# Optimization experiments

Hardware: AMD Instinct MI355X
Metric: run time of the kernel (lower is better)

The kernel has to match this reference:

```python
import jax, jax.numpy as jnp
import numpy as np

N_OER, N_CONCEPT, N_CLASS = 100000, 20000, 1000
F_ENT, HID = 64, 128
E_SR, E_EP, E_COV, E_BEL = 200000, 400000, 400000, 100000
NEG_SLOPE = 0.2


def _edges(k, n_src, n_dst, e):
    k1, k2 = jax.random.split(k)
    return jnp.stack([jax.random.randint(k1, (e,), 0, n_src),
                      jax.random.randint(k2, (e,), 0, n_dst)]).astype(jnp.int32)


def setup_inputs() -> dict:
    key = jax.random.key(0)
    ks = jax.random.split(key, 24)
    s = 0.05  # small init scale for numerically stable attention logits
    inp = {
        'x_oer': jax.random.normal(ks[0], (N_OER, F_ENT), jnp.float32),
        'x_concept': jax.random.normal(ks[1], (N_CONCEPT, F_ENT), jnp.float32),
        'x_class': jax.random.normal(ks[2], (N_CLASS, F_ENT), jnp.float32),
        'e_oer': jax.random.uniform(ks[3], (N_OER, F_ENT), jnp.float32),
        'e_concept': jax.random.uniform(ks[4], (N_CONCEPT, F_ENT), jnp.float32),
        'e_class': jax.random.uniform(ks[5], (N_CLASS, F_ENT), jnp.float32),
        'W_lin': jax.random.normal(ks[6], (3, F_ENT, HID), jnp.float32) * s,
        'b_lin': jnp.zeros((3, HID), jnp.float32),
        'Wsrc': jax.random.normal(ks[7], (2, 5, HID, HID), jnp.float32) * s,
        'Wdst': jax.random.normal(ks[8], (2, 5, HID, HID), jnp.float32) * s,
        'att_src': jax.random.normal(ks[9], (2, 5, HID), jnp.float32) * s,
        'att_dst': jax.random.normal(ks[10], (2, 5, HID), jnp.float32) * s,
        'b_gat': jnp.zeros((2, 5, HID), jnp.float32),
        'W_cls': jax.random.normal(ks[11], (2 * (F_ENT + HID), 1), jnp.float32) * s,
        'b_cls': jnp.zeros((1,), jnp.float32),
        'ei_before_sr': _edges(ks[12], N_OER, N_OER, E_SR),
        'ei_covers': _edges(ks[14], N_OER, N_CONCEPT, E_COV),
        'ei_belongs': _edges(ks[15], N_CONCEPT, N_CLASS, E_BEL),
        'ei_rev_covers': _edges(ks[16], N_CONCEPT, N_OER, E_COV),
        'ei_rev_belongs': _edges(ks[17], N_CLASS, N_CONCEPT, E_BEL),
    }
    # before_ep edges guaranteed self-loop-free (PyG removes then re-adds self loops)
    k1, k2 = jax.random.split(ks[13])
    src = jax.random.randint(k1, (E_EP,), 0, N_OER)
    dst = (src + jax.random.randint(k2, (E_EP,), 1, N_OER)) % N_OER
    inp['ei_before_ep'] = jnp.stack([src, dst]).astype(jnp.int32)
    return inp


def _gat(x_src, x_dst, src, dst, Ws, Wd, a_s, a_d, b, n_dst):
    # PyG GATConv, heads=1: h = xW (no bias); alpha = softmax_dst(leaky_relu(a_s.h_s[i] + a_d.h_d[j]))
    h_s = x_src @ Ws                                   # [Ns, C]
    h_d = x_dst @ Wd                                   # [Nd, C]
    logit = jax.nn.leaky_relu((h_s @ a_s)[src] + (h_d @ a_d)[dst], NEG_SLOPE)  # [E]
    m = jax.ops.segment_max(logit, dst, num_segments=n_dst)
    ex = jnp.exp(logit - m[dst])
    denom = jax.ops.segment_sum(ex, dst, num_segments=n_dst)
    alpha = ex / denom[dst]
    out = jax.ops.segment_sum(h_s[src] * alpha[:, None], dst, num_segments=n_dst)
    return out + b


def _forward(x_oer, x_concept, x_class, e_oer, e_concept, e_class,
             W_lin, b_lin, Wsrc, Wdst, att_src, att_dst, b_gat, W_cls, b_cls,
             ei_before_sr, ei_before_ep, ei_covers, ei_belongs,
             ei_rev_covers, ei_rev_belongs):
    # per-node-type input projection of the random embeddings
    h_oer = e_oer @ W_lin[0] + b_lin[0]
    h_con = e_concept @ W_lin[1] + b_lin[1]
    h_cls = e_class @ W_lin[2] + b_lin[2]

    # add self loops for OER->OER 'before_ep' (add_self_loops=True)
    loop = jnp.arange(N_OER, dtype=jnp.int32)
    ep_src = jnp.concatenate([ei_before_ep[0], loop])
    ep_dst = jnp.concatenate([ei_before_ep[1], loop])

    for l in range(2):
        P = lambda r: (Wsrc[l, r], Wdst[l, r], att_src[l, r], att_dst[l, r], b_gat[l, r])
        o_ep = _gat(h_oer, h_oer, ep_src, ep_dst, *P(0), N_OER)
        o_cov = _gat(h_oer, h_con, ei_covers[0], ei_covers[1], *P(1), N_CONCEPT)
        o_bel = _gat(h_con, h_cls, ei_belongs[0], ei_belongs[1], *P(2), N_CLASS)
        o_rcov = _gat(h_con, h_oer, ei_rev_covers[0], ei_rev_covers[1], *P(3), N_OER)
        o_rbel = _gat(h_cls, h_con, ei_rev_belongs[0], ei_rev_belongs[1], *P(4), N_CONCEPT)
        # HeteroConv aggr='mean' over edge types per destination node type
        h_oer = (o_ep + o_rcov) * 0.5
        h_con = (o_cov + o_rbel) * 0.5
        h_cls = o_bel

    n_oer = jnp.concatenate([x_oer, h_oer], axis=1)          # [N_OER, F_ENT+HID]
    feat = jnp.concatenate([n_oer[ei_before_sr[0]], n_oer[ei_before_sr[1]]], axis=1)
    return (feat @ W_cls + b_cls)[:, 0]                      # [E_SR]


def reference(x_oer, x_concept, x_class, e_oer, e_concept, e_class,
              W_lin, b_lin, Wsrc, Wdst, att_src, att_dst, b_gat, W_cls, b_cls,
              ei_before_sr, ei_before_ep, ei_covers, ei_belongs,
              ei_rev_covers, ei_rev_belongs):
    return _forward(x_oer, x_concept, x_class, e_oer, e_concept, e_class,
                    W_lin, b_lin, Wsrc, Wdst, att_src, att_dst, b_gat, W_cls, b_cls,
                    ei_before_sr, ei_before_ep, ei_covers, ei_belongs,
                    ei_rev_covers, ei_rev_belongs)
```

## Files before the change

### kernel.cpp

```cpp
#include <hip/hip_runtime.h>
#include <hip/hip_bf16.h>

#define NOER 100000
#define NCON 20000
#define NCLS 1000
#define FENT 64
#define HID 128
#define ESR 200000
#define EEP 400000
#define ECOV 400000
#define EBEL 100000
#define NEG 0.2f
#define NB_TOT 121000

#define SL0 0
#define SL1 NOER
#define SL2 (2*NOER)
#define SL3 (2*NOER + NCON)
#define SL4 (2*NOER + 2*NCON)
#define SL_TOT (2*NOER + 2*NCON + NCLS)
#define DL0 0
#define DL1 NOER
#define DL2 (NOER + NCON)
#define DL3 (NOER + NCON + NCLS)
#define DL4 (2*NOER + NCON + NCLS)
#define DL_TOT (2*NOER + 2*NCON + NCLS)
#define EX_TOT 1500000
#define SCAN_B1 ((DL_TOT + 255) / 256)

typedef unsigned short u16;
typedef unsigned int u32;
typedef short v8s __attribute__((ext_vector_type(8)));
typedef float v4f __attribute__((ext_vector_type(4)));

__device__ __forceinline__ float b2f(u32 bits) { return __uint_as_float(bits << 16); }
__device__ __forceinline__ u16 f2b(float x) {
    __hip_bfloat16 h = __float2bfloat16(x);
    return *(u16*)&h;
}
__device__ __forceinline__ float wredsum(float p) {
#pragma unroll
    for (int off = 32; off; off >>= 1) p += __shfl_down(p, off);
    return p;
}

__device__ __forceinline__ void edge_decode(int e, const int* __restrict__ ep,
                                            const int* __restrict__ cov,
                                            const int* __restrict__ bel,
                                            const int* __restrict__ rcov,
                                            const int* __restrict__ rbel,
                                            int& s, int& g) {
    if (e < 500000) {
        if (e < EEP) { s = ep[e]; g = DL0 + ep[EEP + e]; }
        else { s = e - EEP; g = DL0 + s; }
    } else if (e < 900000)  { int i = e - 500000;  s = cov[i];  g = DL1 + cov[ECOV + i]; }
    else if (e < 1000000)   { int i = e - 900000;  s = bel[i];  g = DL2 + bel[EBEL + i]; }
    else if (e < 1400000)   { int i = e - 1000000; s = rcov[i]; g = DL3 + rcov[ECOV + i]; }
    else                    { int i = e - 1400000; s = rbel[i]; g = DL4 + rbel[EBEL + i]; }
}

__global__ void k_count(const int* __restrict__ ep, const int* __restrict__ cov,
                        const int* __restrict__ bel, const int* __restrict__ rcov,
                        const int* __restrict__ rbel, int* __restrict__ counts) {
    int e = blockIdx.x * blockDim.x + threadIdx.x;
    if (e >= EX_TOT) return;
    int s, g;
    edge_decode(e, ep, cov, bel, rcov, rbel, s, g);
    atomicAdd(counts + g, 1);
}

__global__ void k_scan1(const int* __restrict__ counts, int* __restrict__ part,
                        int* __restrict__ bsum) {
    __shared__ int sm[256];
    int i = blockIdx.x * 256 + threadIdx.x;
    int v = (i < DL_TOT) ? counts[i] : 0;
    sm[threadIdx.x] = v;
    __syncthreads();
#pragma unroll
    for (int off = 1; off < 256; off <<= 1) {
        int x = (threadIdx.x >= off) ? sm[threadIdx.x - off] : 0;
        __syncthreads();
        sm[threadIdx.x] += x;
        __syncthreads();
    }
    if (i < DL_TOT) part[i] = sm[threadIdx.x];
    if (threadIdx.x == 255) bsum[blockIdx.x] = sm[255];
}

__global__ void k_scan2(int* __restrict__ bsum) {
    __shared__ int sm[1024];
    int t = threadIdx.x;
    sm[t] = (t < SCAN_B1) ? bsum[t] : 0;
    __syncthreads();
#pragma unroll
    for (int off = 1; off < 1024; off <<= 1) {
        int x = (t >= off) ? sm[t - off] : 0;
        __syncthreads();
        sm[t] += x;
        __syncthreads();
    }
    if (t < SCAN_B1) bsum[t] = sm[t];
}

__global__ void k_scan3(const int* __restrict__ part, const int* __restrict__ bsum,
                        const int* __restrict__ counts, int* __restrict__ S,
                        int* __restrict__ cursor) {
    int i = blockIdx.x * 256 + threadIdx.x;
    if (i >= DL_TOT) return;
    int b = blockIdx.x;
    int s = part[i] + (b > 0 ? bsum[b - 1] : 0);
    S[i] = s;
    cursor[i] = s - counts[i];
}

__global__ void k_fill(const int* __restrict__ ep, const int* __restrict__ cov,
                       const int* __restrict__ bel, const int* __restrict__ rcov,
                       const int* __restrict__ rbel, int* __restrict__ cursor,
                       int* __restrict__ csr) {
    int e = blockIdx.x * blockDim.x + threadIdx.x;
    if (e >= EX_TOT) return;
    int s, g;
    edge_decode(e, ep, cov, bel, rcov, rbel, s, g);
    int pos = atomicAdd(cursor + g, 1);
    csr[pos] = s;
}

__device__ __forceinline__ int deg_bin(int d) { int b = d > 63 ? 63 : d; return 63 - b; }

__global__ void k_hist2(const int* __restrict__ counts, int* __restrict__ bh) {
    __shared__ int lh[64];
    if (threadIdx.x < 64) lh[threadIdx.x] = 0;
    __syncthreads();
    int g = blockIdx.x * 256 + threadIdx.x;
    if (g < DL_TOT) atomicAdd(&lh[deg_bin(counts[g])], 1);
    __syncthreads();
    if (threadIdx.x < 64) bh[threadIdx.x * SCAN_B1 + blockIdx.x] = lh[threadIdx.x];
}

__global__ void k_bscan(const int* __restrict__ bh, int* __restrict__ boff,
                        int* __restrict__ bintot) {
    __shared__ int sm[256];
    __shared__ int carry;
    int bin = blockIdx.x;
    if (threadIdx.x == 0) carry = 0;
    __syncthreads();
    for (int c0 = 0; c0 < SCAN_B1; c0 += 256) {
        int i = c0 + threadIdx.x;
        int v = (i < SCAN_B1) ? bh[bin * SCAN_B1 + i] : 0;
        sm[threadIdx.x] = v;
        __syncthreads();
#pragma unroll
        for (int off = 1; off < 256; off <<= 1) {
            int x = (threadIdx.x >= off) ? sm[threadIdx.x - off] : 0;
            __syncthreads();
            sm[threadIdx.x] += x;
            __syncthreads();
        }
        if (i < SCAN_B1) boff[bin * SCAN_B1 + i] = carry + sm[threadIdx.x] - v;
        __syncthreads();
        if (threadIdx.x == 255) carry += sm[255];
        __syncthreads();
    }
    if (threadIdx.x == 0) bintot[bin] = carry;
}

__global__ void k_hscan(const int* __restrict__ hist, int* __restrict__ bcur) {
    int t = threadIdx.x;
    int h = hist[t];
    int v = h;
#pragma unroll
    for (int off = 1; off < 64; off <<= 1) {
        int x = __shfl_up(v, off);
        if (t >= off) v += x;
    }
    bcur[t] = v - h;
}

__global__ void k_perm2(const int* __restrict__ counts, const int* __restrict__ binbase,
                        const int* __restrict__ boff, int* __restrict__ perm) {
    __shared__ int lh[64];
    if (threadIdx.x < 64)
        lh[threadIdx.x] = binbase[threadIdx.x] + boff[threadIdx.x * SCAN_B1 + blockIdx.x];
    __syncthreads();
    int g = blockIdx.x * 256 + threadIdx.x;
    if (g >= DL_TOT) return;
    int pos = atomicAdd(&lh[deg_bin(counts[g])], 1);
    perm[pos] = g;
}

__global__ void k_cast(const float* __restrict__ e_oer, const float* __restrict__ e_con,
                       const float* __restrict__ e_cls, u16* __restrict__ eb) {
    int idx = blockIdx.x * blockDim.x + threadIdx.x;
    int i4 = idx * 4;
    if (i4 >= NB_TOT * FENT) return;
    const float* src;
    if (i4 < 6400000) src = e_oer + i4;
    else if (i4 < 7680000) src = e_con + (i4 - 6400000);
    else src = e_cls + (i4 - 7680000);
    float4 v = *(const float4*)src;
    u16* d = eb + i4;
    d[0] = f2b(v.x); d[1] = f2b(v.y); d[2] = f2b(v.z); d[3] = f2b(v.w);
}

__global__ void k_prep(const float* __restrict__ W_lin, const float* __restrict__ Wsrc,
                       const float* __restrict__ b_gat,
                       u16* __restrict__ Wlt, u16* __restrict__ Woer, u16* __restrict__ Wcon,
                       u16* __restrict__ Wcls, float* __restrict__ boer,
                       float* __restrict__ bcon, float* __restrict__ bcls2) {
    int i = blockIdx.x * 256 + threadIdx.x;
    if (i < 24576) {
        int t = i / 8192, r = i % 8192, c = r >> 6, k = r & 63;
        Wlt[i] = f2b(W_lin[t * 8192 + k * 128 + c]);
        return;
    }
    i -= 24576;
    if (i < 65536) {
        int l = i >> 15, r = i & 32767, c = r >> 8, k2 = r & 255;
        int rel = 5 * l + (k2 < 128 ? 0 : 3), k = k2 & 127;
        Woer[i] = f2b(Wsrc[(size_t)rel * 16384 + k * 128 + c]);
        return;
    }
    i -= 65536;
    if (i < 65536) {
        int l = i >> 15, r = i & 32767, c = r >> 8, k2 = r & 255;
        int rel = 5 * l + (k2 < 128 ? 1 : 4), k = k2 & 127;
        Wcon[i] = f2b(Wsrc[(size_t)rel * 16384 + k * 128 + c]);
        return;
    }
    i -= 65536;
    if (i < 32768) {
        int l = i >> 14, r = i & 16383, c = r >> 7, k = r & 127;
        Wcls[i] = f2b(Wsrc[(size_t)(5 * l + 2) * 16384 + k * 128 + c]);
        return;
    }
    i -= 32768;
    if (i < 256) { int l = i >> 7, c = i & 127;
        boer[i] = 0.5f * (b_gat[(5 * l + 0) * 128 + c] + b_gat[(5 * l + 3) * 128 + c]); return; }
    i -= 256;
    if (i < 256) { int l = i >> 7, c = i & 127;
        bcon[i] = 0.5f * (b_gat[(5 * l + 1) * 128 + c] + b_gat[(5 * l + 4) * 128 + c]); return; }
    i -= 256;
    if (i < 256) { int l = i >> 7, c = i & 127;
        bcls2[i] = b_gat[(5 * l + 2) * 128 + c]; }
}

__global__ void k_wvec(const float* __restrict__ Wsrc, const float* __restrict__ as_,
                       const float* __restrict__ Wdst, const float* __restrict__ ad,
                       float* __restrict__ wsv, float* __restrict__ wdv) {
    int a = blockIdx.x >> 5;
    int r = ((blockIdx.x & 31) << 2) + (threadIdx.x >> 6);
    int lane = threadIdx.x & 63;
    const float *W, *v;
    float* o;
    if (a < 10) { W = Wsrc + (size_t)a * HID * HID; v = as_ + a * HID; o = wsv + a * HID; }
    else { W = Wdst + (size_t)(a - 10) * HID * HID; v = ad + (a - 10) * HID; o = wdv + (a - 10) * HID; }
    float p = W[r * HID + lane] * v[lane] + W[r * HID + 64 + lane] * v[64 + lane];
    p = wredsum(p);
    if (lane == 0) o[r] = p;
}

struct GemmJob {
    const u16* A0;
    const u16* A1;
    const u16* Wt;
    const float* bias;
    float scale;
    int n, K;
    u16* out;
};

__global__ __launch_bounds__(256) void k_mgemm(GemmJob j0, GemmJob j1, GemmJob j2,
                                               int nb0, int nb1) {
    __shared__ u16 lA[64][40];
    __shared__ u16 lB[128][40];
    GemmJob J;
    int b = blockIdx.x;
    if (b < nb0) J = j0;
    else if (b < nb0 + nb1) { J = j1; b -= nb0; }
    else { J = j2; b -= nb0 + nb1; }
    const int row0 = b * 64;
    const int tid = threadIdx.x, lane = tid & 63, w = tid >> 6;
    const int wr = w >> 1, wc = w & 1;
    const int fr = lane & 15, kg = lane >> 4;
    const int astride = J.A1 ? 128 : J.K;
    v4f acc[2][4];
#pragma unroll
    for (int i = 0; i < 2; ++i)
#pragma unroll
        for (int c = 0; c < 4; ++c) acc[i][c] = (v4f){0.f, 0.f, 0.f, 0.f};

    for (int k0 = 0; k0 < J.K; k0 += 32) {
        const u16* Asrc; int kk;
        if (k0 < 128) { Asrc = J.A0; kk = k0; } else { Asrc = J.A1; kk = k0 - 128; }
        __syncthreads();
        {
            int r = tid >> 2, seg = tid & 3;
            int gr = row0 + r;
            uint4 u = make_uint4(0u, 0u, 0u, 0u);
            if (gr < J.n) u = *(const uint4*)(Asrc + (size_t)gr * astride + kk + seg * 8);
            *(uint4*)&lA[r][seg * 8] = u;
        }
#pragma unroll
        for (int i = 0; i < 2; ++i) {
            int m = tid * 2 + i, c = m >> 2, seg = m & 3;
            uint4 u = *(const uint4*)(J.Wt + (size_t)c * J.K + k0 + seg * 8);
            *(uint4*)&lB[c][seg * 8] = u;
        }
        __syncthreads();
        v8s a0 = *(const v8s*)&lA[32 * wr + fr][8 * kg];
        v8s a1 = *(const v8s*)&lA[32 * wr + 16 + fr][8 * kg];
#pragma unroll
        for (int c = 0; c < 4; ++c) {
            v8s bf = *(const v8s*)&lB[64 * wc + 16 * c + fr][8 * kg];
            acc[0][c] = __builtin_amdgcn_mfma_f32_16x16x32_bf16(a0, bf, acc[0][c], 0, 0, 0);
            acc[1][c] = __builtin_amdgcn_mfma_f32_16x16x32_bf16(a1, bf, acc[1][c], 0, 0, 0);
        }
    }
#pragma unroll
    for (int i = 0; i < 2; ++i)
#pragma unroll
        for (int c = 0; c < 4; ++c) {
            int col = 64 * wc + 16 * c + fr;
            float bv = J.bias[col];
#pragma unroll
            for (int jj = 0; jj < 4; ++jj) {
                int gr = row0 + 32 * wr + 16 * i + 4 * kg + jj;
                if (gr < J.n) J.out[(size_t)gr * 128 + col] = f2b(acc[i][c][jj] * J.scale + bv);
            }
        }
}

__global__ void k_dots_all(const u16* __restrict__ hb, const float* __restrict__ wsv,
                           const float* __restrict__ wdv, float* __restrict__ slp,
                           float* __restrict__ dlp, int lb) {
    int t = blockIdx.x * blockDim.x + threadIdx.x;
    int n = t >> 6, lane = t & 63;
    if (n >= NB_TOT) return;
    const u32* h;
    int m;
    const float *v0, *v1, *v2, *v3;
    float *o0, *o1, *o2, *o3;
    if (n < NOER) {
        m = n; h = (const u32*)hb;
        v0 = wsv + (lb + 0) * HID; o0 = slp + SL0 + m;
        v1 = wsv + (lb + 1) * HID; o1 = slp + SL1 + m;
        v2 = wdv + (lb + 0) * HID; o2 = dlp + DL0 + m;
        v3 = wdv + (lb + 3) * HID; o3 = dlp + DL3 + m;
    } else if (n < NOER + NCON) {
        m = n - NOER; h = (const u32*)(hb + (size_t)NOER * HID);
        v0 = wsv + (lb + 2) * HID; o0 = slp + SL2 + m;
        v1 = wsv + (lb + 3) * HID; o1 = slp + SL3 + m;
        v2 = wdv + (lb + 1) * HID; o2 = dlp + DL1 + m;
        v3 = wdv + (lb + 4) * HID; o3 = dlp + DL4 + m;
    } else {
        m = n - NOER - NCON; h = (const u32*)(hb + (size_t)(NOER + NCON) * HID);
        v0 = wsv + (lb + 4) * HID; o0 = slp + SL4 + m;
        v1 = wdv + (lb + 2) * HID; o1 = dlp + DL2 + m;
        v2 = nullptr; o2 = nullptr; v3 = nullptr; o3 = nullptr;
    }
    u32 hu = h[(size_t)m * 64 + lane];
    float h0 = b2f(hu & 0xffffu), h1 = b2f(hu >> 16);
    float p0 = 0.f, p1 = 0.f, p2 = 0.f, p3 = 0.f;
    { float2 a = *(const float2*)(v0 + 2 * lane); p0 = h0 * a.x + h1 * a.y; }
    { float2 a = *(const float2*)(v1 + 2 * lane); p1 = h0 * a.x + h1 * a.y; }
    if (v2) { float2 a = *(const float2*)(v2 + 2 * lane); p2 = h0 * a.x + h1 * a.y; }
    if (v3) { float2 a = *(const float2*)(v3 + 2 * lane); p3 = h0 * a.x + h1 * a.y; }
    p0 = wredsum(p0); p1 = wredsum(p1); p2 = wredsum(p2); p3 = wredsum(p3);
    if (lane == 0) {
        o0[0] = p0; o1[0] = p1;
        if (o2) o2[0] = p2;
        if (o3) o3[0] = p3;
    }
}

__global__ __launch_bounds__(256) void k_agg_all(const int* __restrict__ csr,
                                                 const int* __restrict__ S,
                                                 const int* __restrict__ perm,
                                                 const float* __restrict__ slp,
                                                 const float* __restrict__ dlp,
                                                 const u16* __restrict__ hb,
                                                 u16* __restrict__ tmp) {
    int gi = blockIdx.x * 16 + (threadIdx.x >> 4);
    if (gi >= DL_TOT) return;
    int g = perm[gi];
    int lane = threadIdx.x & 63;
    int ks = lane & 15;
    int grpbase = lane & 48;
    int c4 = ks * 4;
    const u32* h;
    int sb;
    if (g < DL1)      { h = (const u32*)hb; sb = SL0; }
    else if (g < DL2) { h = (const u32*)hb; sb = SL1; }
    else if (g < DL3) { h = (const u32*)(hb + (size_t)NOER * HID); sb = SL2; }
    else if (g < DL4) { h = (const u32*)(hb + (size_t)NOER * HID); sb = SL3; }
    else              { h = (const u32*)(hb + (size_t)(NOER + NCON) * HID); sb = SL4; }
    int beg = (g == 0) ? 0 : S[g - 1];
    int end = S[g];
    float dlv = dlp[g];
    const u32* hc = h + c4;
    float acc[8] = {};
    float denp = 0.f;
    for (int c0 = beg; c0 < end; c0 += 16) {
        int nch = end - c0;
        if (nch > 16) nch = 16;
        int s_l = 0;
        float ex_l = 0.f;
        if (ks < nch) {
            s_l = csr[c0 + ks];
            float lg = slp[sb + s_l] + dlv;
            lg = lg > 0.f ? lg : NEG * lg;
            ex_l = __expf(lg);
            denp += ex_l;
        }
        uint4 hu[16];
#pragma unroll
        for (int j = 0; j < 16; ++j) {
            if (j < nch) {
                int s = __shfl(s_l, grpbase + j);
                hu[j] = *(const uint4*)(hc + ((size_t)s << 6));
            }
        }
#pragma unroll
        for (int j = 0; j < 16; ++j) {
            if (j < nch) {
                float ex = __shfl(ex_l, grpbase + j);
#pragma unroll
                for (int q = 0; q < 4; ++q) {
                    u32 w = ((const u32*)&hu[j])[q];
                    acc[2 * q]     = fmaf(ex, __uint_as_float(w << 16), acc[2 * q]);
                    acc[2 * q + 1] = fmaf(ex, __uint_as_float(w & 0xffff0000u), acc[2 * q + 1]);
                }
            }
        }
    }
    denp += __shfl_xor(denp, 8);
    denp += __shfl_xor(denp, 4);
    denp += __shfl_xor(denp, 2);
    denp += __shfl_xor(denp, 1);
    float inv = (end > beg) ? 1.f / denp : 0.f;
    uint4 r;
    r.x = (u32)f2b(acc[0] * inv) | ((u32)f2b(acc[1] * inv) << 16);
    r.y = (u32)f2b(acc[2] * inv) | ((u32)f2b(acc[3] * inv) << 16);
    r.z = (u32)f2b(acc[4] * inv) | ((u32)f2b(acc[5] * inv) << 16);
    r.w = (u32)f2b(acc[6] * inv) | ((u32)f2b(acc[7] * inv) << 16);
    *(uint4*)((u32*)tmp + (size_t)g * 64 + c4) = r;
}

__global__ void k_score(const float* __restrict__ x, const u16* __restrict__ hb,
                        const float* __restrict__ Wc, float* __restrict__ s1,
                        float* __restrict__ s2) {
    int t = blockIdx.x * blockDim.x + threadIdx.x;
    int n = t >> 6, lane = t & 63;
    if (n >= NOER) return;
    float xv = x[(size_t)n * FENT + lane];
    u32 hu = ((const u32*)hb)[(size_t)n * 64 + lane];
    float h0 = b2f(hu & 0xffffu), h1 = b2f(hu >> 16);
    float2 wa = *(const float2*)(Wc + 64 + 2 * lane);
    float2 wb = *(const float2*)(Wc + 256 + 2 * lane);
    float p1 = xv * Wc[lane] + h0 * wa.x + h1 * wa.y;
    float p2 = xv * Wc[192 + lane] + h0 * wb.x + h1 * wb.y;
#pragma unroll
    for (int off = 32; off; off >>= 1) { p1 += __shfl_down(p1, off); p2 += __shfl_down(p2, off); }
    if (lane == 0) { s1[n] = p1; s2[n] = p2; }
}

__global__ void k_final(const int* __restrict__ src, const int* __restrict__ dst,
                        const float* __restrict__ s1, const float* __restrict__ s2,
                        const float* __restrict__ bcls, float* __restrict__ out) {
    int e = blockIdx.x * blockDim.x + threadIdx.x;
    if (e >= ESR) return;
    out[e] = s1[src[e]] + s2[dst[e]] + bcls[0];
}

extern "C" void kernel_launch(void* const* d_in, const int* in_sizes, int n_in,
                              void* d_out, int out_size, void* d_ws, size_t ws_size,
                              hipStream_t stream) {
    const float* x_oer   = (const float*)d_in[0];
    const float* e_oer   = (const float*)d_in[3];
    const float* e_con   = (const float*)d_in[4];
    const float* e_cls   = (const float*)d_in[5];
    const float* W_lin   = (const float*)d_in[6];
    const float* b_lin   = (const float*)d_in[7];
    const float* Wsrc    = (const float*)d_in[8];
    const float* Wdst    = (const float*)d_in[9];
    const float* att_src = (const float*)d_in[10];
    const float* att_dst = (const float*)d_in[11];
    const float* b_gat   = (const float*)d_in[12];
    const float* W_cls   = (const float*)d_in[13];
    const float* b_cls   = (const float*)d_in[14];
    const int* ei_sr   = (const int*)d_in[15];
    const int* ei_cov  = (const int*)d_in[16];
    const int* ei_bel  = (const int*)d_in[17];
    const int* ei_rcov = (const int*)d_in[18];
    const int* ei_rbel = (const int*)d_in[19];
    const int* ei_ep   = (const int*)d_in[20];

    float* ws = (float*)d_ws;
    size_t o = 0;
    u16* hb  = (u16*)(ws + o); o += (size_t)NB_TOT * HID / 2;
    u16* eb  = (u16*)(ws + o); o += (size_t)NB_TOT * FENT / 2;
    u16* tmp = (u16*)(ws + o); o += (size_t)DL_TOT * HID / 2;
    float* slp  = ws + o; o += SL_TOT;
    float* dlp  = ws + o; o += DL_TOT;
    float* wsv  = ws + o; o += 10 * HID;
    float* wdv  = ws + o; o += 10 * HID;
    u16* Wlt  = (u16*)(ws + o); o += 3 * HID * FENT / 2;
    u16* Woer = (u16*)(ws + o); o += 2 * HID * 256 / 2;
    u16* Wcon = (u16*)(ws + o); o += 2 * HID * 256 / 2;
    u16* Wcls = (u16*)(ws + o); o += 2 * HID * HID / 2;
    float* boerb = ws + o; o += 2 * HID;
    float* bconb = ws + o; o += 2 * HID;
    float* bcls2 = ws + o; o += 2 * HID;
    float* s1 = ws + o; o += NOER;
    float* s2 = ws + o; o += NOER;
    int* counts = (int*)(ws + o); o += DL_TOT;
    int* part   = (int*)(ws + o); o += DL_TOT;
    int* S      = (int*)(ws + o); o += DL_TOT;
    int* cursor = (int*)(ws + o); o += DL_TOT;
    int* perm   = (int*)(ws + o); o += DL_TOT;
    int* bsum   = (int*)(ws + o); o += 1024;
    int* bh     = (int*)(ws + o); o += 64 * SCAN_B1;
    int* boff   = (int*)(ws + o); o += 64 * SCAN_B1;
    int* bintot = (int*)(ws + o); o += 64;
    int* binbase= (int*)(ws + o); o += 64;
    int* csr    = (int*)(ws + o); o += EX_TOT;

    u16* hb_con = hb + (size_t)NOER * HID;
    u16* hb_cls = hb + (size_t)(NOER + NCON) * HID;

    hipMemsetAsync(counts, 0, DL_TOT * sizeof(int), stream);
    k_count<<<(EX_TOT + 255) / 256, 256, 0, stream>>>(ei_ep, ei_cov, ei_bel, ei_rcov, ei_rbel, counts);
    k_scan1<<<SCAN_B1, 256, 0, stream>>>(counts, part, bsum);
    k_scan2<<<1, 1024, 0, stream>>>(bsum);
    k_scan3<<<SCAN_B1, 256, 0, stream>>>(part, bsum, counts, S, cursor);
    k_hist2<<<SCAN_B1, 256, 0, stream>>>(counts, bh);
    k_bscan<<<64, 256, 0, stream>>>(bh, boff, bintot);
    k_hscan<<<1, 64, 0, stream>>>(bintot, binbase);
    k_perm2<<<SCAN_B1, 256, 0, stream>>>(counts, binbase, boff, perm);
    k_fill<<<(EX_TOT + 255) / 256, 256, 0, stream>>>(ei_ep, ei_cov, ei_bel, ei_rcov, ei_rbel, cursor, csr);

    k_prep<<<739, 256, 0, stream>>>(W_lin, Wsrc, b_gat, Wlt, Woer, Wcon, Wcls, boerb, bconb, bcls2);
    k_cast<<<(NB_TOT * FENT / 4 + 255) / 256, 256, 0, stream>>>(e_oer, e_con, e_cls, eb);
    k_wvec<<<640, 256, 0, stream>>>(Wsrc, att_src, Wdst, att_dst, wsv, wdv);

    {
        GemmJob ja = {eb, nullptr, Wlt, b_lin, 1.f, NOER, FENT, hb};
        GemmJob jb = {eb + (size_t)NOER * FENT, nullptr, Wlt + 8192, b_lin + 128, 1.f, NCON, FENT, hb_con};
        GemmJob jc = {eb + (size_t)(NOER + NCON) * FENT, nullptr, Wlt + 16384, b_lin + 256, 1.f, NCLS, FENT, hb_cls};
        k_mgemm<<<1563 + 313 + 16, 256, 0, stream>>>(ja, jb, jc, 1563, 313);
    }

    for (int l = 0; l < 2; ++l) {
        int lb = l * 5;
        k_dots_all<<<NB_TOT * 64 / 256, 256, 0, stream>>>(hb, wsv, wdv, slp, dlp, lb);
        k_agg_all<<<(DL_TOT + 15) / 16, 256, 0, stream>>>(csr, S, perm, slp, dlp, hb, tmp);
        GemmJob ja = {tmp + (size_t)DL0 * HID, tmp + (size_t)DL3 * HID,
                      Woer + l * 32768, boerb + l * HID, 0.5f, NOER, 256, hb};
        GemmJob jb = {tmp + (size_t)DL1 * HID, tmp + (size_t)DL4 * HID,
                      Wcon + l * 32768, bconb + l * HID, 0.5f, NCON, 256, hb_con};
        GemmJob jc = {tmp + (size_t)DL2 * HID, nullptr,
                      Wcls + l * 16384, bcls2 + l * HID, 1.f, NCLS, 128, hb_cls};
        k_mgemm<<<1563 + 313 + 16, 256, 0, stream>>>(ja, jb, jc, 1563, 313);
    }

    k_score<<<(NOER * 64 + 255) / 256, 256, 0, stream>>>(x_oer, hb, W_cls, s1, s2);
    k_final<<<(ESR + 255) / 256, 256, 0, stream>>>(ei_sr, ei_sr + ESR, s1, s2, b_cls, (float*)d_out);
}
```

Measured before the change: 499.0 us.

## Build CSR via two-pass bucketed fill and drop degree-sorted permutation

Replaces the global-atomic CSR fill with a two-level bucket sort: per-block bucket histograms, a scan of bucket offsets, a block-local scatter of (src,dst) pairs into buckets, and then a per-bucket fill that uses shared-memory cursors. This is meant to localize atomics and scattered writes. It also removes the degree-binned permutation, so aggregation processes destinations in natural order and the four perm-building kernels go away. In exchange, an extra pass writes and reads an intermediate pairs buffer, and aggregation loses its degree-based load balancing. Note that k_fill2 advances the cursor values in shared memory only, so the global cursor array that k_agg_all later reads as row begin stays at the row starts.

```diff
diff --git a/kernel.cpp b/kernel.cpp
--- a/kernel.cpp
+++ b/kernel.cpp
@@ -28,6 +28,12 @@
 #define EX_TOT 1500000
 #define SCAN_B1 ((DL_TOT + 255) / 256)
 
+#define BSH 9
+#define BWID (1 << BSH)
+#define NBUCK ((DL_TOT + BWID - 1) / BWID)
+#define EPB 8192
+#define ABLK ((EX_TOT + EPB - 1) / EPB)
+
 typedef unsigned short u16;
 typedef unsigned int u32;
 typedef short v8s __attribute__((ext_vector_type(8)));
@@ -59,14 +65,25 @@
     else                    { int i = e - 1400000; s = rbel[i]; g = DL4 + rbel[EBEL + i]; }
 }
 
-__global__ void k_count(const int* __restrict__ ep, const int* __restrict__ cov,
-                        const int* __restrict__ bel, const int* __restrict__ rcov,
-                        const int* __restrict__ rbel, int* __restrict__ counts) {
-    int e = blockIdx.x * blockDim.x + threadIdx.x;
-    if (e >= EX_TOT) return;
-    int s, g;
-    edge_decode(e, ep, cov, bel, rcov, rbel, s, g);
-    atomicAdd(counts + g, 1);
+__global__ __launch_bounds__(256) void k_cntA(const int* __restrict__ ep, const int* __restrict__ cov,
+                                              const int* __restrict__ bel, const int* __restrict__ rcov,
+                                              const int* __restrict__ rbel, int* __restrict__ counts,
+                                              int* __restrict__ bhm) {
+    __shared__ int lh[NBUCK];
+    for (int i = threadIdx.x; i < NBUCK; i += 256) lh[i] = 0;
+    __syncthreads();
+    int e0 = blockIdx.x * EPB;
+    for (int k = 0; k < EPB; k += 256) {
+        int e = e0 + k + threadIdx.x;
+        if (e < EX_TOT) {
+            int s, g;
+            edge_decode(e, ep, cov, bel, rcov, rbel, s, g);
+            atomicAdd(counts + g, 1);
+            atomicAdd(&lh[g >> BSH], 1);
+        }
+    }
+    __syncthreads();
+    for (int i = threadIdx.x; i < NBUCK; i += 256) bhm[i * ABLK + blockIdx.x] = lh[i];
 }
 
 __global__ void k_scan1(const int* __restrict__ counts, int* __restrict__ part,
@@ -113,79 +130,58 @@
     cursor[i] = s - counts[i];
 }
 
-__global__ void k_fill(const int* __restrict__ ep, const int* __restrict__ cov,
-                       const int* __restrict__ bel, const int* __restrict__ rcov,
-                       const int* __restrict__ rbel, int* __restrict__ cursor,
-                       int* __restrict__ csr) {
-    int e = blockIdx.x * blockDim.x + threadIdx.x;
-    if (e >= EX_TOT) return;
-    int s, g;
-    edge_decode(e, ep, cov, bel, rcov, rbel, s, g);
-    int pos = atomicAdd(cursor + g, 1);
-    csr[pos] = s;
-}
-
-__device__ __forceinline__ int deg_bin(int d) { int b = d > 63 ? 63 : d; return 63 - b; }
-
-__global__ void k_hist2(const int* __restrict__ counts, int* __restrict__ bh) {
-    __shared__ int lh[64];
-    if (threadIdx.x < 64) lh[threadIdx.x] = 0;
-    __syncthreads();
-    int g = blockIdx.x * 256 + threadIdx.x;
-    if (g < DL_TOT) atomicAdd(&lh[deg_bin(counts[g])], 1);
-    __syncthreads();
-    if (threadIdx.x < 64) bh[threadIdx.x * SCAN_B1 + blockIdx.x] = lh[threadIdx.x];
-}
-
-__global__ void k_bscan(const int* __restrict__ bh, int* __restrict__ boff,
-                        int* __restrict__ bintot) {
+__global__ void k_bscanA(const int* __restrict__ bhm, const int* __restrict__ cursor,
+                         int* __restrict__ starts) {
     __shared__ int sm[256];
-    __shared__ int carry;
-    int bin = blockIdx.x;
-    if (threadIdx.x == 0) carry = 0;
-    __syncthreads();
-    for (int c0 = 0; c0 < SCAN_B1; c0 += 256) {
-        int i = c0 + threadIdx.x;
-        int v = (i < SCAN_B1) ? bh[bin * SCAN_B1 + i] : 0;
-        sm[threadIdx.x] = v;
-        __syncthreads();
-#pragma unroll
-        for (int off = 1; off < 256; off <<= 1) {
-            int x = (threadIdx.x >= off) ? sm[threadIdx.x - off] : 0;
-            __syncthreads();
-            sm[threadIdx.x] += x;
-            __syncthreads();
-        }
-        if (i < SCAN_B1) boff[bin * SCAN_B1 + i] = carry + sm[threadIdx.x] - v;
-        __syncthreads();
-        if (threadIdx.x == 255) carry += sm[255];
-        __syncthreads();
-    }
-    if (threadIdx.x == 0) bintot[bin] = carry;
-}
-
-__global__ void k_hscan(const int* __restrict__ hist, int* __restrict__ bcur) {
-    int t = threadIdx.x;
-    int h = hist[t];
-    int v = h;
-#pragma unroll
-    for (int off = 1; off < 64; off <<= 1) {
-        int x = __shfl_up(v, off);
-        if (t >= off) v += x;
-    }
-    bcur[t] = v - h;
-}
-
-__global__ void k_perm2(const int* __restrict__ counts, const int* __restrict__ binbase,
-                        const int* __restrict__ boff, int* __restrict__ perm) {
-    __shared__ int lh[64];
-    if (threadIdx.x < 64)
-        lh[threadIdx.x] = binbase[threadIdx.x] + boff[threadIdx.x * SCAN_B1 + blockIdx.x];
-    __syncthreads();
-    int g = blockIdx.x * 256 + threadIdx.x;
-    if (g >= DL_TOT) return;
-    int pos = atomicAdd(&lh[deg_bin(counts[g])], 1);
-    perm[pos] = g;
+    int u = blockIdx.x, t = threadIdx.x;
+    int v = (t < ABLK) ? bhm[u * ABLK + t] : 0;
+    sm[t] = v;
+    __syncthreads();
+#pragma unroll
+    for (int off = 1; off < 256; off <<= 1) {
+        int x = (t >= off) ? sm[t - off] : 0;
+        __syncthreads();
+        sm[t] += x;
+        __syncthreads();
+    }
+    if (t < ABLK) starts[u * ABLK + t] = cursor[u << BSH] + sm[t] - v;
+}
+
+__global__ __launch_bounds__(256) void k_bfillA(const int* __restrict__ ep, const int* __restrict__ cov,
+                                                const int* __restrict__ bel, const int* __restrict__ rcov,
+                                                const int* __restrict__ rbel,
+                                                const int* __restrict__ starts, uint2* __restrict__ pairs) {
+    __shared__ int lh[NBUCK];
+    for (int i = threadIdx.x; i < NBUCK; i += 256) lh[i] = starts[i * ABLK + blockIdx.x];
+    __syncthreads();
+    int e0 = blockIdx.x * EPB;
+    for (int k = 0; k < EPB; k += 256) {
+        int e = e0 + k + threadIdx.x;
+        if (e < EX_TOT) {
+            int s, g;
+            edge_decode(e, ep, cov, bel, rcov, rbel, s, g);
+            int pos = atomicAdd(&lh[g >> BSH], 1);
+            pairs[pos] = make_uint2((u32)s, (u32)g);
+        }
+    }
+}
+
+__global__ __launch_bounds__(256) void k_fill2(const uint2* __restrict__ pairs,
+                                               const int* __restrict__ cursor,
+                                               int* __restrict__ csr) {
+    __shared__ int lc[BWID];
+    int u = blockIdx.x;
+    int g0 = u << BSH;
+    int gn = DL_TOT - g0; if (gn > BWID) gn = BWID;
+    for (int i = threadIdx.x; i < gn; i += 256) lc[i] = cursor[g0 + i];
+    __syncthreads();
+    int rb = cursor[g0];
+    int re = (g0 + BWID >= DL_TOT) ? EX_TOT : cursor[g0 + BWID];
+    for (int i = rb + threadIdx.x; i < re; i += 256) {
+        uint2 p = pairs[i];
+        int pos = atomicAdd(&lc[p.y - g0], 1);
+        csr[pos] = (int)p.x;
+    }
 }
 
 __global__ void k_cast(const float* __restrict__ e_oer, const float* __restrict__ e_con,
@@ -375,14 +371,13 @@
 
 __global__ __launch_bounds__(256) void k_agg_all(const int* __restrict__ csr,
                                                  const int* __restrict__ S,
-                                                 const int* __restrict__ perm,
+                                                 const int* __restrict__ cursor,
                                                  const float* __restrict__ slp,
                                                  const float* __restrict__ dlp,
                                                  const u16* __restrict__ hb,
                                                  u16* __restrict__ tmp) {
-    int gi = blockIdx.x * 16 + (threadIdx.x >> 4);
-    if (gi >= DL_TOT) return;
-    int g = perm[gi];
+    int g = blockIdx.x * 16 + (threadIdx.x >> 4);
+    if (g >= DL_TOT) return;
     int lane = threadIdx.x & 63;
     int ks = lane & 15;
     int grpbase = lane & 48;
@@ -394,7 +389,7 @@
     else if (g < DL3) { h = (const u32*)(hb + (size_t)NOER * HID); sb = SL2; }
     else if (g < DL4) { h = (const u32*)(hb + (size_t)NOER * HID); sb = SL3; }
     else              { h = (const u32*)(hb + (size_t)(NOER + NCON) * HID); sb = SL4; }
-    int beg = (g == 0) ? 0 : S[g - 1];
+    int beg = cursor[g];
     int end = S[g];
     float dlv = dlp[g];
     const u32* hc = h + c4;
@@ -517,27 +512,23 @@
     int* part   = (int*)(ws + o); o += DL_TOT;
     int* S      = (int*)(ws + o); o += DL_TOT;
     int* cursor = (int*)(ws + o); o += DL_TOT;
-    int* perm   = (int*)(ws + o); o += DL_TOT;
     int* bsum   = (int*)(ws + o); o += 1024;
-    int* bh     = (int*)(ws + o); o += 64 * SCAN_B1;
-    int* boff   = (int*)(ws + o); o += 64 * SCAN_B1;
-    int* bintot = (int*)(ws + o); o += 64;
-    int* binbase= (int*)(ws + o); o += 64;
+    int* bhm    = (int*)(ws + o); o += NBUCK * ABLK;
+    int* starts = (int*)(ws + o); o += NBUCK * ABLK;
+    uint2* pairs = (uint2*)(ws + o); o += (size_t)EX_TOT * 2;
     int* csr    = (int*)(ws + o); o += EX_TOT;
 
     u16* hb_con = hb + (size_t)NOER * HID;
     u16* hb_cls = hb + (size_t)(NOER + NCON) * HID;
 
     hipMemsetAsync(counts, 0, DL_TOT * sizeof(int), stream);
-    k_count<<<(EX_TOT + 255) / 256, 256, 0, stream>>>(ei_ep, ei_cov, ei_bel, ei_rcov, ei_rbel, counts);
+    k_cntA<<<ABLK, 256, 0, stream>>>(ei_ep, ei_cov, ei_bel, ei_rcov, ei_rbel, counts, bhm);
     k_scan1<<<SCAN_B1, 256, 0, stream>>>(counts, part, bsum);
     k_scan2<<<1, 1024, 0, stream>>>(bsum);
     k_scan3<<<SCAN_B1, 256, 0, stream>>>(part, bsum, counts, S, cursor);
-    k_hist2<<<SCAN_B1, 256, 0, stream>>>(counts, bh);
-    k_bscan<<<64, 256, 0, stream>>>(bh, boff, bintot);
-    k_hscan<<<1, 64, 0, stream>>>(bintot, binbase);
-    k_perm2<<<SCAN_B1, 256, 0, stream>>>(counts, binbase, boff, perm);
-    k_fill<<<(EX_TOT + 255) / 256, 256, 0, stream>>>(ei_ep, ei_cov, ei_bel, ei_rcov, ei_rbel, cursor, csr);
+    k_bscanA<<<NBUCK, 256, 0, stream>>>(bhm, cursor, starts);
+    k_bfillA<<<ABLK, 256, 0, stream>>>(ei_ep, ei_cov, ei_bel, ei_rcov, ei_rbel, starts, pairs);
+    k_fill2<<<NBUCK, 256, 0, stream>>>(pairs, cursor, csr);
 
     k_prep<<<739, 256, 0, stream>>>(W_lin, Wsrc, b_gat, Wlt, Woer, Wcon, Wcls, boerb, bconb, bcls2);
     k_cast<<<(NB_TOT * FENT / 4 + 255) / 256, 256, 0, stream>>>(e_oer, e_con, e_cls, eb);
@@ -553,7 +544,7 @@
     for (int l = 0; l < 2; ++l) {
         int lb = l * 5;
         k_dots_all<<<NB_TOT * 64 / 256, 256, 0, stream>>>(hb, wsv, wdv, slp, dlp, lb);
-        k_agg_all<<<(DL_TOT + 15) / 16, 256, 0, stream>>>(csr, S, perm, slp, dlp, hb, tmp);
+        k_agg_all<<<(DL_TOT + 15) / 16, 256, 0, stream>>>(csr, S, cursor, slp, dlp, hb, tmp);
         GemmJob ja = {tmp + (size_t)DL0 * HID, tmp + (size_t)DL3 * HID,
                       Woer + l * 32768, boerb + l * HID, 0.5f, NOER, 256, hb};
         GemmJob jb = {tmp + (size_t)DL1 * HID, tmp + (size_t)DL4 * HID,
```

Measured after the change: 534.3 us. 1.07x slower.

## Build CSR via two-pass bucketed scatter and precompute permuted segment bounds

Applied to the files above, without the earlier changes.

Replaces the single-pass atomic CSR fill with a two-level bucket sort. Edges are first scattered into 512-destination buckets using per-block shared-memory offsets, then each bucket is placed into the CSR with shared-memory atomics. This is meant to cut global atomic contention and the randomness of the scatter writes. It also stores segment begin and end offsets in permuted order, so the aggregation kernel reads them contiguously instead of gathering from S. The cost is extra kernels and a pairs buffer, plus one more global read and write pass over the edges.

```diff
diff --git a/kernel.cpp b/kernel.cpp
--- a/kernel.cpp
+++ b/kernel.cpp
@@ -28,6 +28,12 @@
 #define EX_TOT 1500000
 #define SCAN_B1 ((DL_TOT + 255) / 256)
 
+#define BSH 9
+#define BWID (1 << BSH)
+#define NBUCK ((DL_TOT + BWID - 1) / BWID)
+#define EPB 4096
+#define ABLK ((EX_TOT + EPB - 1) / EPB)
+
 typedef unsigned short u16;
 typedef unsigned int u32;
 typedef short v8s __attribute__((ext_vector_type(8)));
@@ -59,14 +65,25 @@
     else                    { int i = e - 1400000; s = rbel[i]; g = DL4 + rbel[EBEL + i]; }
 }
 
-__global__ void k_count(const int* __restrict__ ep, const int* __restrict__ cov,
-                        const int* __restrict__ bel, const int* __restrict__ rcov,
-                        const int* __restrict__ rbel, int* __restrict__ counts) {
-    int e = blockIdx.x * blockDim.x + threadIdx.x;
-    if (e >= EX_TOT) return;
-    int s, g;
-    edge_decode(e, ep, cov, bel, rcov, rbel, s, g);
-    atomicAdd(counts + g, 1);
+__global__ __launch_bounds__(256) void k_cntA(const int* __restrict__ ep, const int* __restrict__ cov,
+                                              const int* __restrict__ bel, const int* __restrict__ rcov,
+                                              const int* __restrict__ rbel, int* __restrict__ counts,
+                                              int* __restrict__ bhm) {
+    __shared__ int lh[NBUCK];
+    for (int i = threadIdx.x; i < NBUCK; i += 256) lh[i] = 0;
+    __syncthreads();
+    int e0 = blockIdx.x * EPB;
+    for (int k = 0; k < EPB; k += 256) {
+        int e = e0 + k + threadIdx.x;
+        if (e < EX_TOT) {
+            int s, g;
+            edge_decode(e, ep, cov, bel, rcov, rbel, s, g);
+            atomicAdd(counts + g, 1);
+            atomicAdd(&lh[g >> BSH], 1);
+        }
+    }
+    __syncthreads();
+    for (int i = threadIdx.x; i < NBUCK; i += 256) bhm[i * ABLK + blockIdx.x] = lh[i];
 }
 
 __global__ void k_scan1(const int* __restrict__ counts, int* __restrict__ part,
@@ -113,16 +130,68 @@
     cursor[i] = s - counts[i];
 }
 
-__global__ void k_fill(const int* __restrict__ ep, const int* __restrict__ cov,
-                       const int* __restrict__ bel, const int* __restrict__ rcov,
-                       const int* __restrict__ rbel, int* __restrict__ cursor,
-                       int* __restrict__ csr) {
-    int e = blockIdx.x * blockDim.x + threadIdx.x;
-    if (e >= EX_TOT) return;
-    int s, g;
-    edge_decode(e, ep, cov, bel, rcov, rbel, s, g);
-    int pos = atomicAdd(cursor + g, 1);
-    csr[pos] = s;
+__global__ void k_bscanA(const int* __restrict__ bhm, const int* __restrict__ cursor,
+                         int* __restrict__ starts) {
+    __shared__ int sm[256];
+    __shared__ int carry;
+    int u = blockIdx.x, t = threadIdx.x;
+    if (t == 0) carry = 0;
+    __syncthreads();
+    int base = cursor[u << BSH];
+    for (int c0 = 0; c0 < ABLK; c0 += 256) {
+        int i = c0 + t;
+        int v = (i < ABLK) ? bhm[u * ABLK + i] : 0;
+        sm[t] = v;
+        __syncthreads();
+#pragma unroll
+        for (int off = 1; off < 256; off <<= 1) {
+            int x = (t >= off) ? sm[t - off] : 0;
+            __syncthreads();
+            sm[t] += x;
+            __syncthreads();
+        }
+        if (i < ABLK) starts[u * ABLK + i] = base + carry + sm[t] - v;
+        __syncthreads();
+        if (t == 255) carry += sm[255];
+        __syncthreads();
+    }
+}
+
+__global__ __launch_bounds__(256) void k_bfillA(const int* __restrict__ ep, const int* __restrict__ cov,
+                                                const int* __restrict__ bel, const int* __restrict__ rcov,
+                                                const int* __restrict__ rbel,
+                                                const int* __restrict__ starts, u32* __restrict__ pairs) {
+    __shared__ int lh[NBUCK];
+    for (int i = threadIdx.x; i < NBUCK; i += 256) lh[i] = starts[i * ABLK + blockIdx.x];
+    __syncthreads();
+    int e0 = blockIdx.x * EPB;
+    for (int k = 0; k < EPB; k += 256) {
+        int e = e0 + k + threadIdx.x;
+        if (e < EX_TOT) {
+            int s, g;
+            edge_decode(e, ep, cov, bel, rcov, rbel, s, g);
+            int pos = atomicAdd(&lh[g >> BSH], 1);
+            pairs[pos] = ((u32)s << BSH) | (u32)(g & (BWID - 1));
+        }
+    }
+}
+
+__global__ __launch_bounds__(256) void k_fill2(const u32* __restrict__ pairs,
+                                               const int* __restrict__ cursor,
+                                               int* __restrict__ csr) {
+    __shared__ int lc[BWID];
+    int u = blockIdx.x;
+    int g0 = u << BSH;
+    int gn = DL_TOT - g0; if (gn > BWID) gn = BWID;
+    for (int i = threadIdx.x; i < gn; i += 256) lc[i] = cursor[g0 + i];
+    __syncthreads();
+    int rb = cursor[g0];
+    int re = (g0 + BWID >= DL_TOT) ? EX_TOT : cursor[g0 + BWID];
+    for (int i = rb + threadIdx.x; i < re; i += 256) {
+        u32 p = pairs[i];
+        int pos = atomicAdd(&lc[p & (BWID - 1)], 1);
+        csr[pos] = (int)(p >> BSH);
+    }
 }
 
 __device__ __forceinline__ int deg_bin(int d) { int b = d > 63 ? 63 : d; return 63 - b; }
@@ -177,7 +246,9 @@
 }
 
 __global__ void k_perm2(const int* __restrict__ counts, const int* __restrict__ binbase,
-                        const int* __restrict__ boff, int* __restrict__ perm) {
+                        const int* __restrict__ boff, const int* __restrict__ cursor,
+                        const int* __restrict__ S, int* __restrict__ perm,
+                        int* __restrict__ segbeg, int* __restrict__ segend) {
     __shared__ int lh[64];
     if (threadIdx.x < 64)
         lh[threadIdx.x] = binbase[threadIdx.x] + boff[threadIdx.x * SCAN_B1 + blockIdx.x];
@@ -186,6 +257,8 @@
     if (g >= DL_TOT) return;
     int pos = atomicAdd(&lh[deg_bin(counts[g])], 1);
     perm[pos] = g;
+    segbeg[pos] = cursor[g];
+    segend[pos] = S[g];
 }
 
 __global__ void k_cast(const float* __restrict__ e_oer, const float* __restrict__ e_con,
@@ -374,8 +447,9 @@
 }
 
 __global__ __launch_bounds__(256) void k_agg_all(const int* __restrict__ csr,
-                                                 const int* __restrict__ S,
                                                  const int* __restrict__ perm,
+                                                 const int* __restrict__ segbeg,
+                                                 const int* __restrict__ segend,
                                                  const float* __restrict__ slp,
                                                  const float* __restrict__ dlp,
                                                  const u16* __restrict__ hb,
@@ -383,6 +457,8 @@
     int gi = blockIdx.x * 16 + (threadIdx.x >> 4);
     if (gi >= DL_TOT) return;
     int g = perm[gi];
+    int beg = segbeg[gi];
+    int end = segend[gi];
     int lane = threadIdx.x & 63;
     int ks = lane & 15;
     int grpbase = lane & 48;
@@ -394,8 +470,6 @@
     else if (g < DL3) { h = (const u32*)(hb + (size_t)NOER * HID); sb = SL2; }
     else if (g < DL4) { h = (const u32*)(hb + (size_t)NOER * HID); sb = SL3; }
     else              { h = (const u32*)(hb + (size_t)(NOER + NCON) * HID); sb = SL4; }
-    int beg = (g == 0) ? 0 : S[g - 1];
-    int end = S[g];
     float dlv = dlp[g];
     const u32* hc = h + c4;
     float acc[8] = {};
@@ -518,26 +592,33 @@
     int* S      = (int*)(ws + o); o += DL_TOT;
     int* cursor = (int*)(ws + o); o += DL_TOT;
     int* perm   = (int*)(ws + o); o += DL_TOT;
+    int* segbeg = (int*)(ws + o); o += DL_TOT;
+    int* segend = (int*)(ws + o); o += DL_TOT;
     int* bsum   = (int*)(ws + o); o += 1024;
+    int* bhm    = (int*)(ws + o); o += NBUCK * ABLK;
+    int* starts = (int*)(ws + o); o += NBUCK * ABLK;
     int* bh     = (int*)(ws + o); o += 64 * SCAN_B1;
     int* boff   = (int*)(ws + o); o += 64 * SCAN_B1;
     int* bintot = (int*)(ws + o); o += 64;
     int* binbase= (int*)(ws + o); o += 64;
+    u32* pairs  = (u32*)(ws + o); o += EX_TOT;
     int* csr    = (int*)(ws + o); o += EX_TOT;
 
     u16* hb_con = hb + (size_t)NOER * HID;
     u16* hb_cls = hb + (size_t)(NOER + NCON) * HID;
 
     hipMemsetAsync(counts, 0, DL_TOT * sizeof(int), stream);
-    k_count<<<(EX_TOT + 255) / 256, 256, 0, stream>>>(ei_ep, ei_cov, ei_bel, ei_rcov, ei_rbel, counts);
+    k_cntA<<<ABLK, 256, 0, stream>>>(ei_ep, ei_cov, ei_bel, ei_rcov, ei_rbel, counts, bhm);
     k_scan1<<<SCAN_B1, 256, 0, stream>>>(counts, part, bsum);
     k_scan2<<<1, 1024, 0, stream>>>(bsum);
     k_scan3<<<SCAN_B1, 256, 0, stream>>>(part, bsum, counts, S, cursor);
+    k_bscanA<<<NBUCK, 256, 0, stream>>>(bhm, cursor, starts);
+    k_bfillA<<<ABLK, 256, 0, stream>>>(ei_ep, ei_cov, ei_bel, ei_rcov, ei_rbel, starts, pairs);
+    k_fill2<<<NBUCK, 256, 0, stream>>>(pairs, cursor, csr);
     k_hist2<<<SCAN_B1, 256, 0, stream>>>(counts, bh);
     k_bscan<<<64, 256, 0, stream>>>(bh, boff, bintot);
     k_hscan<<<1, 64, 0, stream>>>(bintot, binbase);
-    k_perm2<<<SCAN_B1, 256, 0, stream>>>(counts, binbase, boff, perm);
-    k_fill<<<(EX_TOT + 255) / 256, 256, 0, stream>>>(ei_ep, ei_cov, ei_bel, ei_rcov, ei_rbel, cursor, csr);
+    k_perm2<<<SCAN_B1, 256, 0, stream>>>(counts, binbase, boff, cursor, S, perm, segbeg, segend);
 
     k_prep<<<739, 256, 0, stream>>>(W_lin, Wsrc, b_gat, Wlt, Woer, Wcon, Wcls, boerb, bconb, bcls2);
     k_cast<<<(NB_TOT * FENT / 4 + 255) / 256, 256, 0, stream>>>(e_oer, e_con, e_cls, eb);
@@ -553,7 +634,7 @@
     for (int l = 0; l < 2; ++l) {
         int lb = l * 5;
         k_dots_all<<<NB_TOT * 64 / 256, 256, 0, stream>>>(hb, wsv, wdv, slp, dlp, lb);
-        k_agg_all<<<(DL_TOT + 15) / 16, 256, 0, stream>>>(csr, S, perm, slp, dlp, hb, tmp);
+        k_agg_all<<<(DL_TOT + 15) / 16, 256, 0, stream>>>(csr, perm, segbeg, segend, slp, dlp, hb, tmp);
         GemmJob ja = {tmp + (size_t)DL0 * HID, tmp + (size_t)DL3 * HID,
                       Woer + l * 32768, boerb + l * HID, 0.5f, NOER, 256, hb};
         GemmJob jb = {tmp + (size_t)DL1 * HID, tmp + (size_t)DL4 * HID,
```

New measurement: 501.3 us. About the same (+0.5%).
